# Kernel optimization log

Hardware: AMD Instinct MI355X
Metric: run time of the kernel (lower is better)

Reference implementation:

```python
import jax, jax.numpy as jnp
import numpy as np

B = 2          # batch size
T2 = 9         # temporal groups (b*t2 = grid_sample batch)
T3 = 27        # t1 // t2
T1 = 243       # t2 * t3
P = 17         # joints
K2 = 9         # kernel_size ** 2
C = 128        # dim_img
CH = [48, 96, 192, 384]
HW = [(96, 72), (48, 36), (24, 18), (12, 9)]
ALPHA = 0.9


def setup_inputs() -> dict:
    key = jax.random.key(0)
    ks = jax.random.split(key, 16)
    inp = {}
    N = B * T2
    for i, (c, (h, w)) in enumerate(zip(CH, HW)):
        inp[f"f{i}"] = jax.random.normal(ks[i], (N, c, h, w), jnp.float32)
    inp["query"] = jax.random.normal(ks[4], (B, T1, P * K2, C), jnp.float32)
    # key holds normalized grid coords in [-1, 1]
    inp["key"] = jax.random.uniform(ks[5], (N, T3, P * K2, 2), jnp.float32) * 2.0 - 1.0
    inp["value"] = jax.random.normal(ks[6], (B, T1, P, C), jnp.float32)
    s = 0.05
    inp["w_off"] = jax.random.normal(ks[7], (2, C), jnp.float32) * s
    inp["b_off"] = jnp.zeros((2,), jnp.float32)
    inp["w_attn"] = jax.random.normal(ks[8], (2, C), jnp.float32) * s
    inp["b_attn"] = jnp.zeros((2,), jnp.float32)
    for i, c in enumerate(CH):
        inp[f"we{i}"] = jax.random.normal(ks[9 + i], (C, c), jnp.float32) * s
        inp[f"be{i}"] = jnp.zeros((C,), jnp.float32)
    inp["conv_w"] = jax.random.normal(ks[13], (C, C, K2), jnp.float32) * s
    inp["conv_b"] = jnp.zeros((C,), jnp.float32)
    return inp


def _grid_sample(img, grid):
    """Bilinear grid_sample, align_corners=False, zero padding.
    img: [N, C, H, W]; grid: [N, Hg, Wg, 2] in [-1,1] (x=width, y=height).
    Returns [N, Hg, Wg, C] (channels-last for the following 1x1 conv)."""
    N, Cin, H, W = img.shape
    gx, gy = grid[..., 0], grid[..., 1]
    ix = ((gx + 1.0) * W - 1.0) * 0.5
    iy = ((gy + 1.0) * H - 1.0) * 0.5
    ix0 = jnp.floor(ix); iy0 = jnp.floor(iy)
    wx1 = ix - ix0; wx0 = 1.0 - wx1
    wy1 = iy - iy0; wy0 = 1.0 - wy1
    bidx = jnp.arange(N)[:, None, None]

    def gather(yy, xx):
        yi = yy.astype(jnp.int32); xi = xx.astype(jnp.int32)
        valid = (yi >= 0) & (yi < H) & (xi >= 0) & (xi < W)
        yc = jnp.clip(yi, 0, H - 1); xc = jnp.clip(xi, 0, W - 1)
        v = img[bidx, :, yc, xc]  # [N, Hg, Wg, C]
        return v * valid[..., None].astype(img.dtype)

    out = (gather(iy0, ix0) * (wy0 * wx0)[..., None]
           + gather(iy0, ix0 + 1.0) * (wy0 * wx1)[..., None]
           + gather(iy0 + 1.0, ix0) * (wy1 * wx0)[..., None]
           + gather(iy0 + 1.0, ix0 + 1.0) * (wy1 * wx1)[..., None])
    return out


def reference(f0, f1, f2, f3, query, key, value,
              w_off, b_off, w_attn, b_attn,
              we0, be0, we1, be1, we2, be2, we3, be3,
              conv_w, conv_b):
    b, t1, p, c = value.shape            # [B, 243, 17, 128]
    t3 = key.shape[1]                    # 27
    t2 = t1 // t3                        # 9

    # learned offsets per query location, squashed by tanh
    off = jnp.tanh(jnp.einsum('btqc,oc->btqo', query, w_off) + b_off)   # [b,t1,153,2]
    # per-joint softmax weights, tiled over the k^2 kernel taps
    aw = jax.nn.softmax(jnp.einsum('btpc,oc->btpo', value, w_attn) + b_attn, axis=-1)  # [b,t1,17,2]
    aw = jnp.tile(aw, (1, 1, K2, 1))                                     # [b,t1,153,2]

    sp = (off * aw).reshape(b * t2, t3, p * K2, 2)
    sampling_positions = key + sp                                        # [b*t2, 27, 153, 2]

    fmaps = (f0, f1, f2, f3)
    ws = (we0, we1, we2, we3)
    bs = (be0, be1, be2, be3)
    feats = []
    for f, w, bb in zip(fmaps, ws, bs):
        g = _grid_sample(f, sampling_positions)                          # [b*t2, 27, 153, C_in]
        e = jnp.einsum('nhwc,oc->nhwo', g, w) + bb                        # 1x1 conv embed -> 128
        feats.append(e.reshape(b, t2 * t3, p * K2, C))                    # [b, 243, 153, 128]
    new_query = jnp.mean(jnp.stack(feats, axis=-2), axis=-2)             # fuse 4 levels
    new_query = (1.0 - ALPHA) * new_query + ALPHA * query

    # grouped-by-position conv1d over the k^2 taps (full-width kernel -> length 1)
    x = new_query.reshape(b, t1, p, K2, c)                               # 'b t (p k) c'
    new_value = jnp.einsum('btpkc,ock->btpo', x, conv_w) + conv_b        # [b, 243, 17, 128]
    return (new_query, new_value, sampling_positions)
```

## Files before the change

kernel.cpp:

```cpp
#include <hip/hip_runtime.h>
#include <hip/hip_bf16.h>

static constexpr int NQ_SIZE = 9517824;
static constexpr int NV_SIZE = 1057536;
static constexpr int NPOS    = 74358;
static constexpr int M_CONV  = 8262;

static constexpr long E0_OFF = 0;
static constexpr long E1_OFF = 15925248;
static constexpr long E2_OFF = E1_OFF + 3981312;
static constexpr long E3_OFF = E2_OFF + 995328;
static constexpr long E_END  = E3_OFF + 248832;

static constexpr int SEG_F3  = 36;
static constexpr int SEG_F2  = SEG_F3 + 126;
static constexpr int SEG_F1  = SEG_F2 + 486;
static constexpr int SEG_F0  = SEG_F1 + 1944;
static constexpr int SEG_CT  = SEG_F0 + 576;
static constexpr int SEG_SP  = SEG_CT + 486;
static constexpr int PREP_GRID = SEG_SP;

typedef __attribute__((ext_vector_type(8))) short short8;
typedef __attribute__((ext_vector_type(4))) float floatx4;

__device__ __forceinline__ float bf2f(unsigned short u) {
    union { unsigned int i; float f; } v; v.i = ((unsigned)u) << 16; return v.f;
}
__device__ __forceinline__ unsigned short f2bf_rne(float f) {
    union { float f; unsigned int i; } v; v.f = f;
    unsigned int u = v.i;
    u += 0x7fffu + ((u >> 16) & 1u);
    return (unsigned short)(u >> 16);
}
__device__ __forceinline__ short8 pack8(const float* t) {
    union { unsigned short u[8]; short8 s; } r;
    #pragma unroll
    for (int i = 0; i < 8; ++i) r.u[i] = f2bf_rne(t[i]);
    return r.s;
}

__global__ __launch_bounds__(256) void prep_k(
    const float* __restrict__ f0, const float* __restrict__ f1,
    const float* __restrict__ f2, const float* __restrict__ f3,
    const float* __restrict__ we0, const float* __restrict__ we1,
    const float* __restrict__ we2, const float* __restrict__ we3,
    const float* __restrict__ conv_w, unsigned short* __restrict__ convT2,
    const float* __restrict__ query, const float* __restrict__ value,
    const float* __restrict__ key,
    const float* __restrict__ w_off, const float* __restrict__ b_off,
    const float* __restrict__ w_attn, const float* __restrict__ b_attn,
    float* __restrict__ samp, unsigned short* __restrict__ Ebase)
{
    const int bid = blockIdx.x;
    const int tid = threadIdx.x;

    if (bid < SEG_F0) {
        __shared__ unsigned short Bs[128][40];

        const float* A; const float* W; unsigned short* Eo;
        int M, K, m0;
        if (bid < SEG_F3) {
            int n = bid >> 1, t = bid & 1;
            M = 108; K = 384; A = f3 + (long)n * 384 * 108; W = we3;
            Eo = Ebase + E3_OFF + (long)n * 108 * 128; m0 = t * 64;
        } else if (bid < SEG_F2) {
            int r = bid - SEG_F3; int n = r / 7, t = r - n * 7;
            M = 432; K = 192; A = f2 + (long)n * 192 * 432; W = we2;
            Eo = Ebase + E2_OFF + (long)n * 432 * 128; m0 = t * 64;
        } else if (bid < SEG_F1) {
            int r = bid - SEG_F2; int n = r / 27, t = r - n * 27;
            M = 1728; K = 96; A = f1 + (long)n * 96 * 1728; W = we1;
            Eo = Ebase + E1_OFF + (long)n * 1728 * 128; m0 = t * 64;
        } else {
            int r = bid - SEG_F1; int n = r / 108, t = r - n * 108;
            M = 6912; K = 48; A = f0 + (long)n * 48 * 6912; W = we0;
            Eo = Ebase + E0_OFF + (long)n * 6912 * 128; m0 = t * 64;
        }

        const int lane = tid & 63;
        const int wave = tid >> 6;
        const int l15  = lane & 15;
        const int quad = lane >> 4;
        const int mg   = m0 + wave * 16 + l15;

        floatx4 acc[8];
        #pragma unroll
        for (int j = 0; j < 8; ++j) acc[j] = (floatx4){0.f, 0.f, 0.f, 0.f};

        const int sbo = tid >> 1;
        const int sbk = (tid & 1) << 4;

        float4 bv0, bv1, bv2, bv3;
        auto fetchB = [&](int k0) {
            bv0 = (float4){0,0,0,0}; bv1 = bv0; bv2 = bv0; bv3 = bv0;
            if (k0 + sbk < K) {
                const float* wp = W + (long)sbo * K + k0 + sbk;
                bv0 = *(const float4*)wp;
                bv1 = *(const float4*)(wp + 4);
                bv2 = *(const float4*)(wp + 8);
                bv3 = *(const float4*)(wp + 12);
            }
        };
        fetchB(0);

        for (int k0 = 0; k0 < K; k0 += 32) {
            float a_f[8];
            {
                const int kq = k0 + quad * 8;
                const float* ap = A + (long)kq * M + mg;
                #pragma unroll
                for (int j = 0; j < 8; ++j) {
                    a_f[j] = 0.f;
                    if (mg < M && kq + j < K) a_f[j] = ap[(long)j * M];
                }
            }
            {
                float tmp[16] = {bv0.x, bv0.y, bv0.z, bv0.w, bv1.x, bv1.y, bv1.z, bv1.w,
                                 bv2.x, bv2.y, bv2.z, bv2.w, bv3.x, bv3.y, bv3.z, bv3.w};
                unsigned short t[16];
                #pragma unroll
                for (int i = 0; i < 16; ++i) t[i] = f2bf_rne(tmp[i]);
                *(uint4*)&Bs[sbo][sbk]     = *(const uint4*)&t[0];
                *(uint4*)&Bs[sbo][sbk + 8] = *(const uint4*)&t[8];
            }
            __syncthreads();
            if (k0 + 32 < K) fetchB(k0 + 32);

            short8 af = pack8(a_f);
            #pragma unroll
            for (int nt = 0; nt < 8; ++nt) {
                short8 bf = *(const short8*)&Bs[nt * 16 + l15][quad * 8];
                acc[nt] = __builtin_amdgcn_mfma_f32_16x16x32_bf16(af, bf, acc[nt], 0, 0, 0);
            }
            __syncthreads();
        }

        #pragma unroll
        for (int nt = 0; nt < 8; ++nt) {
            int col = nt * 16 + l15;
            #pragma unroll
            for (int r = 0; r < 4; ++r) {
                int m = m0 + wave * 16 + quad * 4 + r;
                if (m < M)
                    Eo[(long)m * 128 + col] = f2bf_rne(acc[nt][r]);
            }
        }
    } else if (bid < SEG_CT) {
        int idx = (bid - SEG_F0) * 256 + tid;
        if (idx < 147456) {
            int o = idx / 1152, kk = idx - o * 1152;
            int k2 = kk >> 7, c = kk & 127;
            convT2[idx] = f2bf_rne(conv_w[o * 1152 + c * 9 + k2]);
        }
    } else {
        const int bt1 = bid - SEG_CT;
        const int b  = bt1 / 243, t1 = bt1 - b * 243;
        const int t2 = t1 / 27,  t3 = t1 - t2 * 27;
        const int n  = b * 9 + t2;
        __shared__ float logit[17][2];
        __shared__ float aw[17][2];

        if (tid < 34) {
            int p = tid >> 1, o = tid & 1;
            const float* vrow = value + ((long)bt1 * 17 + p) * 128;
            const float* wrow = w_attn + o * 128;
            float s = 0.f;
            for (int c = 0; c < 128; c += 4) {
                float4 v = *(const float4*)(vrow + c);
                float4 w = *(const float4*)(wrow + c);
                s += v.x * w.x + v.y * w.y + v.z * w.z + v.w * w.w;
            }
            logit[p][o] = s + b_attn[o];
        }
        __syncthreads();
        if (tid < 17) {
            float l0 = logit[tid][0], l1 = logit[tid][1];
            float mx = fmaxf(l0, l1);
            float e0 = expf(l0 - mx), e1 = expf(l1 - mx);
            float inv = 1.f / (e0 + e1);
            aw[tid][0] = e0 * inv; aw[tid][1] = e1 * inv;
        }
        __syncthreads();
        for (int j = tid; j < 306; j += 256) {
            int q = j >> 1, o = j & 1;
            const float* qrow = query + ((long)bt1 * 153 + q) * 128;
            const float* wrow = w_off + o * 128;
            float s = 0.f;
            for (int c = 0; c < 128; c += 4) {
                float4 v = *(const float4*)(qrow + c);
                float4 w = *(const float4*)(wrow + c);
                s += v.x * w.x + v.y * w.y + v.z * w.z + v.w * w.w;
            }
            float off = tanhf(s + b_off[o]);
            float sp = off * aw[q % 17][o];
            long kidx = (((long)n * 27 + t3) * 153 + q) * 2 + o;
            samp[kidx] = key[kidx] + sp;
        }
    }
}

__global__ __launch_bounds__(256) void gather_k(
    const unsigned short* __restrict__ Ebase,
    const float* __restrict__ samp, const float* __restrict__ query,
    const float* __restrict__ be0, const float* __restrict__ be1,
    const float* __restrict__ be2, const float* __restrict__ be3,
    float* __restrict__ nq)
{
    const int tid = threadIdx.x;
    const int pos = blockIdx.x * 8 + (tid >> 5);
    if (pos >= NPOS) return;
    const int c4 = (tid & 31) << 2;
    const int bt1 = pos / 153, q = pos - bt1 * 153;
    const int b  = bt1 / 243, t1 = bt1 - b * 243;
    const int t2 = t1 / 27,  t3 = t1 - t2 * 27;
    const int n  = b * 9 + t2;
    const long sbase = (((long)n * 27 + t3) * 153 + q) * 2;
    const float gx = samp[sbase], gy = samp[sbase + 1];

    float ax = 0.f, ay = 0.f, az = 0.f, aww = 0.f;
    const long Eoffs[4] = {E0_OFF, E1_OFF, E2_OFF, E3_OFF};
    const int Hs[4] = {96, 48, 24, 12}, Wd[4] = {72, 36, 18, 9};
    #pragma unroll
    for (int l = 0; l < 4; ++l) {
        const int H = Hs[l], W = Wd[l];
        const unsigned short* E = Ebase + Eoffs[l] + (long)n * H * W * 128 + c4;
        float ix = ((gx + 1.f) * (float)W - 1.f) * 0.5f;
        float iy = ((gy + 1.f) * (float)H - 1.f) * 0.5f;
        float fx0 = floorf(ix), fy0 = floorf(iy);
        int x0 = (int)fx0, y0 = (int)fy0;
        int x1 = x0 + 1, y1 = y0 + 1;
        float wx1 = ix - fx0, wx0 = 1.f - wx1;
        float wy1 = iy - fy0, wy0 = 1.f - wy1;
        float w00 = wy0 * wx0, w01 = wy0 * wx1, w10 = wy1 * wx0, w11 = wy1 * wx1;
        bool vy0 = (unsigned)y0 < (unsigned)H, vy1 = (unsigned)y1 < (unsigned)H;
        bool vx0 = (unsigned)x0 < (unsigned)W, vx1 = (unsigned)x1 < (unsigned)W;
        if (vy0 && vx0) { ushort4 v = *(const ushort4*)(E + ((long)y0 * W + x0) * 128);
            ax = fmaf(w00, bf2f(v.x), ax); ay = fmaf(w00, bf2f(v.y), ay);
            az = fmaf(w00, bf2f(v.z), az); aww = fmaf(w00, bf2f(v.w), aww); }
        if (vy0 && vx1) { ushort4 v = *(const ushort4*)(E + ((long)y0 * W + x1) * 128);
            ax = fmaf(w01, bf2f(v.x), ax); ay = fmaf(w01, bf2f(v.y), ay);
            az = fmaf(w01, bf2f(v.z), az); aww = fmaf(w01, bf2f(v.w), aww); }
        if (vy1 && vx0) { ushort4 v = *(const ushort4*)(E + ((long)y1 * W + x0) * 128);
            ax = fmaf(w10, bf2f(v.x), ax); ay = fmaf(w10, bf2f(v.y), ay);
            az = fmaf(w10, bf2f(v.z), az); aww = fmaf(w10, bf2f(v.w), aww); }
        if (vy1 && vx1) { ushort4 v = *(const ushort4*)(E + ((long)y1 * W + x1) * 128);
            ax = fmaf(w11, bf2f(v.x), ax); ay = fmaf(w11, bf2f(v.y), ay);
            az = fmaf(w11, bf2f(v.z), az); aww = fmaf(w11, bf2f(v.w), aww); }
    }
    float bsx = be0[c4]     + be1[c4]     + be2[c4]     + be3[c4];
    float bsy = be0[c4 + 1] + be1[c4 + 1] + be2[c4 + 1] + be3[c4 + 1];
    float bsz = be0[c4 + 2] + be1[c4 + 2] + be2[c4 + 2] + be3[c4 + 2];
    float bsw = be0[c4 + 3] + be1[c4 + 3] + be2[c4 + 3] + be3[c4 + 3];
    float mx = 0.25f * (ax + bsx), my = 0.25f * (ay + bsy);
    float mz = 0.25f * (az + bsz), mw = 0.25f * (aww + bsw);
    const long qi = ((long)bt1 * 153 + q) * 128 + c4;
    float4 qv = *(const float4*)(query + qi);
    float4 o;
    o.x = 0.1f * mx + 0.9f * qv.x;
    o.y = 0.1f * my + 0.9f * qv.y;
    o.z = 0.1f * mz + 0.9f * qv.z;
    o.w = 0.1f * mw + 0.9f * qv.w;
    *(float4*)(nq + qi) = o;
}

__global__ __launch_bounds__(256) void conv_mfma_k(
    const float* __restrict__ nq, const unsigned short* __restrict__ convT2,
    const float* __restrict__ conv_b, float* __restrict__ nv)
{
    __shared__ unsigned short As[32][40];
    __shared__ unsigned short Bs[64][40];

    const int tid  = threadIdx.x;
    const int lane = tid & 63;
    const int wave = tid >> 6;
    const int wm = (wave & 1) * 16;
    const int wn = (wave >> 1) * 32;
    const int m0 = blockIdx.x * 32;
    const int n0 = blockIdx.y * 64;
    const int l15  = lane & 15;
    const int quad = lane >> 4;

    floatx4 acc[2];
    acc[0] = (floatx4){0.f, 0.f, 0.f, 0.f};
    acc[1] = acc[0];

    const int am = tid >> 3;
    const int ak = (tid & 7) << 2;
    const int bn = tid >> 2;
    const int bk = (tid & 3) << 3;

    float4 a0; uint4 bv;
    auto fetch = [&](int k0) {
        a0 = (float4){0,0,0,0};
        int row = m0 + am;
        if (row < M_CONV)
            a0 = *(const float4*)(nq + (long)row * 1152 + k0 + ak);
        bv = *(const uint4*)(convT2 + (long)(n0 + bn) * 1152 + k0 + bk);
    };
    fetch(0);

    for (int k0 = 0; k0 < 1152; k0 += 32) {
        unsigned short t[4] = {f2bf_rne(a0.x), f2bf_rne(a0.y), f2bf_rne(a0.z), f2bf_rne(a0.w)};
        *(uint2*)&As[am][ak] = *(const uint2*)t;
        *(uint4*)&Bs[bn][bk] = bv;
        __syncthreads();
        if (k0 + 32 < 1152) fetch(k0 + 32);

        short8 af = *(const short8*)&As[wm + l15][quad * 8];
        #pragma unroll
        for (int nt = 0; nt < 2; ++nt) {
            short8 bf = *(const short8*)&Bs[wn + nt * 16 + l15][quad * 8];
            acc[nt] = __builtin_amdgcn_mfma_f32_16x16x32_bf16(af, bf, acc[nt], 0, 0, 0);
        }
        __syncthreads();
    }

    #pragma unroll
    for (int nt = 0; nt < 2; ++nt) {
        int col = n0 + wn + nt * 16 + l15;
        float bias = conv_b[col];
        #pragma unroll
        for (int r = 0; r < 4; ++r) {
            int row = m0 + wm + quad * 4 + r;
            if (row < M_CONV)
                nv[(long)row * 128 + col] = acc[nt][r] + bias;
        }
    }
}

extern "C" void kernel_launch(void* const* d_in, const int* in_sizes, int n_in,
                              void* d_out, int out_size, void* d_ws, size_t ws_size,
                              hipStream_t stream) {
    const float* f0     = (const float*)d_in[0];
    const float* f1     = (const float*)d_in[1];
    const float* f2     = (const float*)d_in[2];
    const float* f3     = (const float*)d_in[3];
    const float* query  = (const float*)d_in[4];
    const float* key    = (const float*)d_in[5];
    const float* value  = (const float*)d_in[6];
    const float* w_off  = (const float*)d_in[7];
    const float* b_off  = (const float*)d_in[8];
    const float* w_attn = (const float*)d_in[9];
    const float* b_attn = (const float*)d_in[10];
    const float* we0    = (const float*)d_in[11];
    const float* be0    = (const float*)d_in[12];
    const float* we1    = (const float*)d_in[13];
    const float* be1    = (const float*)d_in[14];
    const float* we2    = (const float*)d_in[15];
    const float* be2    = (const float*)d_in[16];
    const float* we3    = (const float*)d_in[17];
    const float* be3    = (const float*)d_in[18];
    const float* conv_w = (const float*)d_in[19];
    const float* conv_b = (const float*)d_in[20];

    float* out  = (float*)d_out;
    float* nq   = out;
    float* nv   = out + NQ_SIZE;
    float* samp = out + NQ_SIZE + NV_SIZE;

    unsigned short* Ebase  = (unsigned short*)d_ws;
    unsigned short* convT2 = Ebase + E_END;

    prep_k<<<PREP_GRID, 256, 0, stream>>>(
        f0, f1, f2, f3, we0, we1, we2, we3, conv_w, convT2,
        query, value, key, w_off, b_off, w_attn, b_attn, samp, Ebase);

    gather_k<<<(NPOS + 7) / 8, 256, 0, stream>>>(Ebase, samp, query, be0, be1, be2, be3, nq);

    conv_mfma_k<<<dim3(259, 2), 256, 0, stream>>>(nq, convT2, conv_b, nv);
}
```

Baseline: 243.3 us.

## Retile feature projection GEMM to 128-row blocks with chunked K staging

Rewrites the per-level 1x1 projection GEMM in the prep kernel as a templated body. Each wave now computes 32 rows instead of 16, so every block covers 128 rows, and the weight tile is staged into shared memory in K chunks of up to 96 instead of 32. This means fewer barriers and more reuse of each B fragment, and compile-time M/K specialisations drop bounds checks on full tiles. The block segments are also reordered so the long level-3 blocks and the sampling-position blocks are scheduled early. The trade-off is half as many blocks, more accumulator registers per thread and a larger shared-memory footprint.

Result: no change. 240.7 us (-1.1%).

```diff
diff --git a/kernel.cpp b/kernel.cpp
--- a/kernel.cpp
+++ b/kernel.cpp
@@ -12,13 +12,13 @@
 static constexpr long E3_OFF = E2_OFF + 995328;
 static constexpr long E_END  = E3_OFF + 248832;
 
-static constexpr int SEG_F3  = 36;
-static constexpr int SEG_F2  = SEG_F3 + 126;
-static constexpr int SEG_F1  = SEG_F2 + 486;
-static constexpr int SEG_F0  = SEG_F1 + 1944;
-static constexpr int SEG_CT  = SEG_F0 + 576;
-static constexpr int SEG_SP  = SEG_CT + 486;
-static constexpr int PREP_GRID = SEG_SP;
+static constexpr int SEG_L3 = 18;
+static constexpr int SEG_SP = SEG_L3 + 486;
+static constexpr int SEG_L2 = SEG_SP + 72;
+static constexpr int SEG_L1 = SEG_L2 + 252;
+static constexpr int SEG_L0 = SEG_L1 + 972;
+static constexpr int SEG_CT = SEG_L0 + 576;
+static constexpr int PREP_GRID = SEG_CT;
 
 typedef __attribute__((ext_vector_type(8))) short short8;
 typedef __attribute__((ext_vector_type(4))) float floatx4;
@@ -37,6 +37,104 @@
     #pragma unroll
     for (int i = 0; i < 8; ++i) r.u[i] = f2bf_rne(t[i]);
     return r.s;
+}
+
+template<int K, int M, bool FULLM>
+__device__ __forceinline__ void proj_body(
+    const float* __restrict__ A, const float* __restrict__ W,
+    unsigned short* __restrict__ Eo, int m0, int tid,
+    unsigned short (*Bs)[104])
+{
+    constexpr int KC      = (K < 96) ? K : 96;
+    constexpr int KCPAD   = (KC + 31) & ~31;
+    constexpr int KT      = KCPAD / 32;
+    constexpr int NCH     = K / KC;
+    constexpr bool NEEDPAD = (KCPAD != KC);
+
+    const int lane = tid & 63;
+    const int wave = tid >> 6;
+    const int l15  = lane & 15;
+    const int quad = lane >> 4;
+    const int mg0  = m0 + wave * 32 + l15;
+    const int mg1  = mg0 + 16;
+    const bool v0  = FULLM || (mg0 < M);
+    const bool v1  = FULLM || (mg1 < M);
+
+    floatx4 acc[2][8];
+    #pragma unroll
+    for (int f = 0; f < 2; ++f)
+        #pragma unroll
+        for (int nt = 0; nt < 8; ++nt) acc[f][nt] = (floatx4){0.f, 0.f, 0.f, 0.f};
+
+    const int so  = tid >> 1;
+    const int skb = (tid & 1) * (KCPAD / 2);
+
+    #pragma unroll 1
+    for (int ch = 0; ch < NCH; ++ch) {
+        const int kc = ch * KC;
+        if (ch) __syncthreads();
+        {
+            const float* wp = W + (long)so * K + kc + skb;
+            #pragma unroll
+            for (int k = 0; k < KCPAD / 2; k += 8) {
+                float t[8];
+                #pragma unroll
+                for (int j = 0; j < 8; ++j)
+                    t[j] = (!NEEDPAD || (skb + k + j < KC)) ? wp[k + j] : 0.f;
+                unsigned short u[8];
+                #pragma unroll
+                for (int j = 0; j < 8; ++j) u[j] = f2bf_rne(t[j]);
+                *(uint4*)&Bs[so][skb + k] = *(const uint4*)u;
+            }
+        }
+        __syncthreads();
+
+        #pragma unroll
+        for (int kt = 0; kt < KT; ++kt) {
+            const int kg = kc + kt * 32 + quad * 8;
+            float a0[8], a1[8];
+            const float* ap = A + (long)kg * M + mg0;
+            const bool fastk = !NEEDPAD || (kg + 8 <= K);
+            if (FULLM && fastk) {
+                #pragma unroll
+                for (int j = 0; j < 8; ++j) {
+                    a0[j] = ap[(long)j * M];
+                    a1[j] = ap[(long)j * M + 16];
+                }
+            } else {
+                #pragma unroll
+                for (int j = 0; j < 8; ++j) {
+                    a0[j] = 0.f; a1[j] = 0.f;
+                    if (kg + j < K) {
+                        if (v0) a0[j] = ap[(long)j * M];
+                        if (v1) a1[j] = ap[(long)j * M + 16];
+                    }
+                }
+            }
+            short8 af0 = pack8(a0);
+            short8 af1 = pack8(a1);
+            #pragma unroll
+            for (int nt = 0; nt < 8; ++nt) {
+                short8 bf = *(const short8*)&Bs[nt * 16 + l15][kt * 32 + quad * 8];
+                acc[0][nt] = __builtin_amdgcn_mfma_f32_16x16x32_bf16(af0, bf, acc[0][nt], 0, 0, 0);
+                acc[1][nt] = __builtin_amdgcn_mfma_f32_16x16x32_bf16(af1, bf, acc[1][nt], 0, 0, 0);
+            }
+        }
+    }
+
+    #pragma unroll
+    for (int f = 0; f < 2; ++f) {
+        const int rb = m0 + wave * 32 + f * 16 + quad * 4;
+        #pragma unroll
+        for (int nt = 0; nt < 8; ++nt) {
+            const int col = nt * 16 + l15;
+            #pragma unroll
+            for (int r = 0; r < 4; ++r) {
+                if (FULLM || (rb + r < M))
+                    Eo[(long)(rb + r) * 128 + col] = f2bf_rne(acc[f][nt][r]);
+            }
+        }
+    }
 }
 
 __global__ __launch_bounds__(256) void prep_k(
@@ -54,106 +152,32 @@
     const int bid = blockIdx.x;
     const int tid = threadIdx.x;
 
-    if (bid < SEG_F0) {
-        __shared__ unsigned short Bs[128][40];
-
-        const float* A; const float* W; unsigned short* Eo;
-        int M, K, m0;
-        if (bid < SEG_F3) {
-            int n = bid >> 1, t = bid & 1;
-            M = 108; K = 384; A = f3 + (long)n * 384 * 108; W = we3;
-            Eo = Ebase + E3_OFF + (long)n * 108 * 128; m0 = t * 64;
-        } else if (bid < SEG_F2) {
-            int r = bid - SEG_F3; int n = r / 7, t = r - n * 7;
-            M = 432; K = 192; A = f2 + (long)n * 192 * 432; W = we2;
-            Eo = Ebase + E2_OFF + (long)n * 432 * 128; m0 = t * 64;
-        } else if (bid < SEG_F1) {
-            int r = bid - SEG_F2; int n = r / 27, t = r - n * 27;
-            M = 1728; K = 96; A = f1 + (long)n * 96 * 1728; W = we1;
-            Eo = Ebase + E1_OFF + (long)n * 1728 * 128; m0 = t * 64;
+    if (bid < SEG_L3 || (bid >= SEG_SP && bid < SEG_L0)) {
+        __shared__ unsigned short Bs[128][104];
+
+        if (bid < SEG_L3) {
+            int n = bid;
+            proj_body<384, 108, false>(f3 + (long)n * 384 * 108, we3,
+                Ebase + E3_OFF + (long)n * 108 * 128, 0, tid, Bs);
+        } else if (bid < SEG_L2) {
+            int r = bid - SEG_SP; int n = r >> 2, t = r & 3;
+            const float* A = f2 + (long)n * 192 * 432;
+            unsigned short* Eo = Ebase + E2_OFF + (long)n * 432 * 128;
+            if (t < 3) proj_body<192, 432, true >(A, we2, Eo, t * 128, tid, Bs);
+            else       proj_body<192, 432, false>(A, we2, Eo, t * 128, tid, Bs);
+        } else if (bid < SEG_L1) {
+            int r = bid - SEG_L2; int n = r / 14, t = r - n * 14;
+            const float* A = f1 + (long)n * 96 * 1728;
+            unsigned short* Eo = Ebase + E1_OFF + (long)n * 1728 * 128;
+            if (t < 13) proj_body<96, 1728, true >(A, we1, Eo, t * 128, tid, Bs);
+            else        proj_body<96, 1728, false>(A, we1, Eo, t * 128, tid, Bs);
         } else {
-            int r = bid - SEG_F1; int n = r / 108, t = r - n * 108;
-            M = 6912; K = 48; A = f0 + (long)n * 48 * 6912; W = we0;
-            Eo = Ebase + E0_OFF + (long)n * 6912 * 128; m0 = t * 64;
-        }
-
-        const int lane = tid & 63;
-        const int wave = tid >> 6;
-        const int l15  = lane & 15;
-        const int quad = lane >> 4;
-        const int mg   = m0 + wave * 16 + l15;
-
-        floatx4 acc[8];
-        #pragma unroll
-        for (int j = 0; j < 8; ++j) acc[j] = (floatx4){0.f, 0.f, 0.f, 0.f};
-
-        const int sbo = tid >> 1;
-        const int sbk = (tid & 1) << 4;
-
-        float4 bv0, bv1, bv2, bv3;
-        auto fetchB = [&](int k0) {
-            bv0 = (float4){0,0,0,0}; bv1 = bv0; bv2 = bv0; bv3 = bv0;
-            if (k0 + sbk < K) {
-                const float* wp = W + (long)sbo * K + k0 + sbk;
-                bv0 = *(const float4*)wp;
-                bv1 = *(const float4*)(wp + 4);
-                bv2 = *(const float4*)(wp + 8);
-                bv3 = *(const float4*)(wp + 12);
-            }
-        };
-        fetchB(0);
-
-        for (int k0 = 0; k0 < K; k0 += 32) {
-            float a_f[8];
-            {
-                const int kq = k0 + quad * 8;
-                const float* ap = A + (long)kq * M + mg;
-                #pragma unroll
-                for (int j = 0; j < 8; ++j) {
-                    a_f[j] = 0.f;
-                    if (mg < M && kq + j < K) a_f[j] = ap[(long)j * M];
-                }
-            }
-            {
-                float tmp[16] = {bv0.x, bv0.y, bv0.z, bv0.w, bv1.x, bv1.y, bv1.z, bv1.w,
-                                 bv2.x, bv2.y, bv2.z, bv2.w, bv3.x, bv3.y, bv3.z, bv3.w};
-                unsigned short t[16];
-                #pragma unroll
-                for (int i = 0; i < 16; ++i) t[i] = f2bf_rne(tmp[i]);
-                *(uint4*)&Bs[sbo][sbk]     = *(const uint4*)&t[0];
-                *(uint4*)&Bs[sbo][sbk + 8] = *(const uint4*)&t[8];
-            }
-            __syncthreads();
-            if (k0 + 32 < K) fetchB(k0 + 32);
-
-            short8 af = pack8(a_f);
-            #pragma unroll
-            for (int nt = 0; nt < 8; ++nt) {
-                short8 bf = *(const short8*)&Bs[nt * 16 + l15][quad * 8];
-                acc[nt] = __builtin_amdgcn_mfma_f32_16x16x32_bf16(af, bf, acc[nt], 0, 0, 0);
-            }
-            __syncthreads();
-        }
-
-        #pragma unroll
-        for (int nt = 0; nt < 8; ++nt) {
-            int col = nt * 16 + l15;
-            #pragma unroll
-            for (int r = 0; r < 4; ++r) {
-                int m = m0 + wave * 16 + quad * 4 + r;
-                if (m < M)
-                    Eo[(long)m * 128 + col] = f2bf_rne(acc[nt][r]);
-            }
-        }
-    } else if (bid < SEG_CT) {
-        int idx = (bid - SEG_F0) * 256 + tid;
-        if (idx < 147456) {
-            int o = idx / 1152, kk = idx - o * 1152;
-            int k2 = kk >> 7, c = kk & 127;
-            convT2[idx] = f2bf_rne(conv_w[o * 1152 + c * 9 + k2]);
-        }
-    } else {
-        const int bt1 = bid - SEG_CT;
+            int r = bid - SEG_L1; int n = r / 54, t = r - n * 54;
+            proj_body<48, 6912, true>(f0 + (long)n * 48 * 6912, we0,
+                Ebase + E0_OFF + (long)n * 6912 * 128, t * 128, tid, Bs);
+        }
+    } else if (bid < SEG_SP) {
+        const int bt1 = bid - SEG_L3;
         const int b  = bt1 / 243, t1 = bt1 - b * 243;
         const int t2 = t1 / 27,  t3 = t1 - t2 * 27;
         const int n  = b * 9 + t2;
@@ -195,6 +219,13 @@
             float sp = off * aw[q % 17][o];
             long kidx = (((long)n * 27 + t3) * 153 + q) * 2 + o;
             samp[kidx] = key[kidx] + sp;
+        }
+    } else {
+        int idx = (bid - SEG_L0) * 256 + tid;
+        if (idx < 147456) {
+            int o = idx / 1152, kk = idx - o * 1152;
+            int k2 = kk >> 7, c = kk & 127;
+            convT2[idx] = f2bf_rne(conv_w[o * 1152 + c * 9 + k2]);
         }
     }
 }
```
